# Performance work log

Hardware: AMD Instinct MI355X
Metric: run time of the kernel (lower is better)

Reference implementation:

```python
import jax, jax.numpy as jnp
import numpy as np

NUM_HEADS = 12

def setup_inputs() -> dict:
    key = jax.random.key(0)
    k1, k2, k3, k4 = jax.random.split(key, 4)
    B, N, C = 64, 197, 768
    x = jax.random.normal(k1, (B, N, C), dtype=jnp.float32)
    w_qkv = jax.random.normal(k2, (3 * C, C), dtype=jnp.float32) * (C ** -0.5)
    w_proj = jax.random.normal(k3, (C, C), dtype=jnp.float32) * (C ** -0.5)
    b_proj = jax.random.normal(k4, (C,), dtype=jnp.float32) * 0.01
    return {"x": x, "w_qkv": w_qkv, "w_proj": w_proj, "b_proj": b_proj}

def reference(x, w_qkv, w_proj, b_proj):
    B, N, C = x.shape
    H = NUM_HEADS
    hd = C // H
    scale = hd ** -0.5
    # qkv linear (no bias): [B,N,3C] -> [3,B,H,N,hd]
    qkv = jnp.einsum('bnc,dc->bnd', x, w_qkv).reshape(B, N, 3, H, hd)
    qkv = jnp.transpose(qkv, (2, 0, 3, 1, 4))
    q, k, v = qkv[0], qkv[1], qkv[2]
    # full attention matrix [B,H,N,N] (materialized, matching the original)
    attn = jax.nn.softmax(jnp.einsum('bhnd,bhmd->bhnm', q, k) * scale, axis=-1)
    # CLS-token attention stats: mean over heads of attn row 0 (patch tokens) -> [B, N-1]
    global_attn = jnp.mean(attn[:, :, 0, 1:], axis=1)
    out = jnp.einsum('bhnm,bhmd->bhnd', attn, v)          # [B,H,N,hd]
    out = jnp.transpose(out, (0, 2, 1, 3)).reshape(B, N, C)
    out = jnp.einsum('bnc,dc->bnd', out, w_proj) + b_proj
    return out, global_attn
```

## Files before the change

### kernel.cpp

```cpp
#include <hip/hip_runtime.h>
#include <math.h>

#define B_   64
#define N_   197
#define C_   768
#define H_   12
#define HD_  64
#define BH_  (B_ * H_)
#define M_   (B_ * N_)

typedef _Float16 half8 __attribute__((ext_vector_type(8)));
typedef float    f32x4 __attribute__((ext_vector_type(4)));

#define XH_OFF   0u
#define WQH_OFF  19365888u
#define WPH_OFF  22904832u
#define QH_OFF   24084480u
#define KH_OFF   43450368u
#define VH_OFF   62816256u
#define OH_OFF   82182144u
#define P0_OFF   101548032u
#define WS_BYTES 102150144u

__device__ __forceinline__ half8 h8zero() {
    half8 z;
    #pragma unroll
    for (int i = 0; i < 8; ++i) z[i] = (_Float16)0;
    return z;
}

__device__ __forceinline__ void async16(const _Float16* g, _Float16* l) {
    __builtin_amdgcn_global_load_lds(
        (const __attribute__((address_space(1))) void*)g,
        (__attribute__((address_space(3))) void*)l,
        16, 0, 0);
}

__device__ __forceinline__ int xcd_swz(int i, int nwg) {
    const int q = nwg >> 3, r = nwg & 7;
    const int xcd = i & 7, j = i >> 3;
    return (xcd < r ? xcd * (q + 1) : r * (q + 1) + (xcd - r) * q) + j;
}

__global__ void k_ws_too_small(float* out, float ws_bytes) { out[0] = -ws_bytes; }

__global__ __launch_bounds__(256) void k_cvt_all(const float* __restrict__ x,
                                                 const float* __restrict__ wq,
                                                 const float* __restrict__ wp,
                                                 _Float16* __restrict__ Xh,
                                                 _Float16* __restrict__ Wqh,
                                                 _Float16* __restrict__ Wph) {
    int i = blockIdx.x * blockDim.x + threadIdx.x;
    const float* src;
    _Float16*    dst;
    if (i < 1210368)      { src = x;  dst = Xh; }
    else if (i < 1431552) { src = wq; dst = Wqh; i -= 1210368; }
    else                  { src = wp; dst = Wph; i -= 1431552; }
    float4 f0 = *(const float4*)(src + (size_t)i * 8);
    float4 f1 = *(const float4*)(src + (size_t)i * 8 + 4);
    half8 h;
    h[0]=(_Float16)f0.x; h[1]=(_Float16)f0.y; h[2]=(_Float16)f0.z; h[3]=(_Float16)f0.w;
    h[4]=(_Float16)f1.x; h[5]=(_Float16)f1.y; h[6]=(_Float16)f1.z; h[7]=(_Float16)f1.w;
    *(half8*)(dst + (size_t)i * 8) = h;
}

__device__ __forceinline__ void mfma_nt_core_h(const _Float16* __restrict__ A,
                                               const _Float16* __restrict__ B,
                                               int M, int K, int m0, int n0,
                                               _Float16* As, _Float16* Bs,
                                               f32x4 (&acc)[4][4]) {
    const int tid  = threadIdx.x;
    const int wave = tid >> 6, lane = tid & 63;
    const int wr   = (wave >> 1) << 6;
    const int wc   = (wave & 1) << 6;
    const int ln   = lane & 15, kq = lane >> 4;

    const int row0 = tid >> 2;
    const int ch0  = (tid & 3) << 3;
    int ar0 = m0 + row0;        if (ar0 >= M) ar0 = 0;
    int ar1 = m0 + 64 + row0;   if (ar1 >= M) ar1 = 0;
    const _Float16* A0 = A + (size_t)ar0 * K + ch0;
    const _Float16* A1 = A + (size_t)ar1 * K + ch0;
    const _Float16* B0 = B + (size_t)(n0 + row0) * K + ch0;
    const _Float16* B1 = B + (size_t)(n0 + 64 + row0) * K + ch0;
    _Float16* AsD = As + (wave << 9);
    _Float16* BsD = Bs + (wave << 9);

    for (int k0 = 0; k0 < K; k0 += 32) {
        __syncthreads();
        async16(A0 + k0, AsD);
        async16(A1 + k0, AsD + 2048);
        async16(B0 + k0, BsD);
        async16(B1 + k0, BsD + 2048);
        __syncthreads();

        half8 af[4], bf[4];
        #pragma unroll
        for (int t = 0; t < 4; ++t) {
            af[t] = *(const half8*)&As[(wr + t * 16 + ln) * 32 + kq * 8];
            bf[t] = *(const half8*)&Bs[(wc + t * 16 + ln) * 32 + kq * 8];
        }
        #pragma unroll
        for (int i = 0; i < 4; ++i)
            #pragma unroll
            for (int j = 0; j < 4; ++j)
                acc[i][j] = __builtin_amdgcn_mfma_f32_16x16x32_f16(af[i], bf[j], acc[i][j], 0, 0, 0);
    }
}

__global__ __launch_bounds__(256) void k_qkv_mfma(const _Float16* __restrict__ Xh,
                                                  const _Float16* __restrict__ Wq,
                                                  _Float16* __restrict__ Qh,
                                                  _Float16* __restrict__ Kh,
                                                  _Float16* __restrict__ Vh) {
    __shared__ _Float16 As[128 * 32];
    __shared__ _Float16 Bs[128 * 32];
    const int work = xcd_swz(blockIdx.y * 18 + blockIdx.x, 18 * 99);
    const int m0 = (work / 18) << 7;
    const int n0 = (work % 18) << 7;
    f32x4 acc[4][4] = {};
    mfma_nt_core_h(Xh, Wq, M_, C_, m0, n0, As, Bs, acc);

    const int lane = threadIdx.x & 63;
    const int wave = threadIdx.x >> 6;
    const int wr = (wave >> 1) << 6, wc = (wave & 1) << 6;
    const int ln = lane & 15, kq = lane >> 4;

    _Float16* basep[4];
    float     scl[4];
    #pragma unroll
    for (int nt = 0; nt < 4; ++nt) {
        const int d  = n0 + wc + nt * 16 + ln;
        const int t3 = d / C_;
        const int rr = d - t3 * C_;
        const int h  = rr >> 6;
        const int e  = rr & 63;
        _Float16* t = (t3 == 0) ? Qh : (t3 == 1) ? Kh : Vh;
        basep[nt] = t + (size_t)h * N_ * HD_ + e;
        scl[nt]   = (t3 == 0) ? 0.125f : 1.f;
    }
    #pragma unroll
    for (int mt = 0; mt < 4; ++mt) {
        #pragma unroll
        for (int i = 0; i < 4; ++i) {
            const int m = m0 + wr + mt * 16 + kq * 4 + i;
            if (m >= M_) continue;
            const int b = m / N_;
            const int n = m - b * N_;
            const size_t rowoff = ((size_t)b * H_ * N_ + n) * HD_;
            #pragma unroll
            for (int nt = 0; nt < 4; ++nt)
                basep[nt][rowoff] = (_Float16)(acc[mt][nt][i] * scl[nt]);
        }
    }
}

__global__ __launch_bounds__(256) void k_proj_mfma(const _Float16* __restrict__ Oh,
                                                   const _Float16* __restrict__ Wp,
                                                   const float* __restrict__ bias,
                                                   float* __restrict__ out) {
    __shared__ _Float16 As[128 * 32];
    __shared__ _Float16 Bs[128 * 32];
    const int work = xcd_swz(blockIdx.y * 6 + blockIdx.x, 6 * 99);
    const int m0 = (work / 6) << 7;
    const int n0 = (work % 6) << 7;
    f32x4 acc[4][4] = {};
    mfma_nt_core_h(Oh, Wp, M_, C_, m0, n0, As, Bs, acc);

    const int lane = threadIdx.x & 63;
    const int wave = threadIdx.x >> 6;
    const int wr = (wave >> 1) << 6, wc = (wave & 1) << 6;
    const int ln = lane & 15, kq = lane >> 4;
    float bv[4];
    #pragma unroll
    for (int nt = 0; nt < 4; ++nt) bv[nt] = bias[n0 + wc + nt * 16 + ln];
    #pragma unroll
    for (int mt = 0; mt < 4; ++mt) {
        #pragma unroll
        for (int i = 0; i < 4; ++i) {
            const int m = m0 + wr + mt * 16 + kq * 4 + i;
            if (m >= M_) continue;
            #pragma unroll
            for (int nt = 0; nt < 4; ++nt)
                out[(size_t)m * C_ + n0 + wc + nt * 16 + ln] = acc[mt][nt][i] + bv[nt];
        }
    }
}

__global__ __launch_bounds__(256) void k_attn(const _Float16* __restrict__ Qh,
                                              const _Float16* __restrict__ Kh,
                                              const _Float16* __restrict__ Vh,
                                              _Float16* __restrict__ Oh,
                                              float* __restrict__ P0) {
    __shared__ _Float16 lds[29824];
    _Float16* Ks = lds;
    _Float16* Pl = lds;
    _Float16* Vt = lds + 14976;

    const int work = xcd_swz(blockIdx.y * 4 + blockIdx.x, 4 * BH_);
    const int bh = work >> 2, rt = work & 3;
    const int b = bh / H_, h = bh - b * H_;
    const int tid = threadIdx.x, wave = tid >> 6, lane = tid & 63;
    const int ln = lane & 15, kq = lane >> 4;
    const size_t kvb = (size_t)bh * N_ * HD_;

    for (int idx = tid; idx < 208 * 8; idx += 256) {
        const int key = idx >> 3, c = (idx & 7) << 3;
        half8 v = (key < N_) ? *(const half8*)(Kh + kvb + (size_t)key * HD_ + c) : h8zero();
        *(half8*)&Ks[key * 72 + c] = v;
    }
    for (int idx = tid; idx < 197 * 8; idx += 256) {
        const int key = idx >> 3, c = (idx & 7) << 3;
        half8 v = *(const half8*)(Vh + kvb + (size_t)key * HD_ + c);
        #pragma unroll
        for (int j = 0; j < 8; ++j) Vt[(c + j) * 232 + key] = v[j];
    }
    for (int idx = tid; idx < 64 * 27; idx += 256) {
        const int d = idx / 27, k = 197 + (idx - d * 27);
        Vt[d * 232 + k] = (_Float16)0;
    }
    const int qrow = rt * 64 + wave * 16 + ln;
    const _Float16* Qp = Qh + kvb + (size_t)((qrow < N_) ? qrow : 0) * HD_ + kq * 8;
    half8 qf0 = *(const half8*)Qp;
    half8 qf1 = *(const half8*)(Qp + 32);
    __syncthreads();

    f32x4 acc[13] = {};
    __builtin_amdgcn_s_setprio(1);
    #pragma unroll
    for (int c = 0; c < 13; ++c) {
        const _Float16* kp = &Ks[(c * 16 + ln) * 72 + kq * 8];
        half8 kf0 = *(const half8*)kp;
        half8 kf1 = *(const half8*)(kp + 32);
        acc[c] = __builtin_amdgcn_mfma_f32_16x16x32_f16(qf0, kf0, acc[c], 0, 0, 0);
        acc[c] = __builtin_amdgcn_mfma_f32_16x16x32_f16(qf1, kf1, acc[c], 0, 0, 0);
    }
    __builtin_amdgcn_s_setprio(0);
    float inv4[4];
    #pragma unroll
    for (int r = 0; r < 4; ++r) {
        float m = -1e30f;
        #pragma unroll
        for (int c = 0; c < 13; ++c) {
            float x = ((c * 16 + ln) < N_) ? acc[c][r] : -1e30f;
            acc[c][r] = x;
            m = fmaxf(m, x);
        }
        m = fmaxf(m, __shfl_xor(m, 1)); m = fmaxf(m, __shfl_xor(m, 2));
        m = fmaxf(m, __shfl_xor(m, 4)); m = fmaxf(m, __shfl_xor(m, 8));
        float s = 0.f;
        #pragma unroll
        for (int c = 0; c < 13; ++c) { float e = __expf(acc[c][r] - m); acc[c][r] = e; s += e; }
        s += __shfl_xor(s, 1); s += __shfl_xor(s, 2);
        s += __shfl_xor(s, 4); s += __shfl_xor(s, 8);
        inv4[r] = 1.f / s;
    }
    __syncthreads();

    _Float16* Pw = Pl + wave * 16 * 232;
    #pragma unroll
    for (int c = 0; c < 13; ++c) {
        const int col = c * 16 + ln;
        #pragma unroll
        for (int r = 0; r < 4; ++r)
            Pw[(kq * 4 + r) * 232 + col] = (_Float16)(acc[c][r] * inv4[r]);
    }
    #pragma unroll
    for (int r = 0; r < 4; ++r) Pw[(kq * 4 + r) * 232 + 208 + ln] = (_Float16)0;

    if (rt == 0 && wave == 0 && kq == 0) {
        #pragma unroll
        for (int c = 0; c < 13; ++c) {
            const int col = c * 16 + ln;
            if (col >= 1 && col < N_) P0[(size_t)bh * 196 + col - 1] = acc[c][0] * inv4[0];
        }
    }
    __syncthreads();

    f32x4 o4[4] = {};
    __builtin_amdgcn_s_setprio(1);
    for (int t = 0; t < 7; ++t) {
        half8 pf = *(const half8*)&Pw[ln * 232 + kq * 8 + 32 * t];
        #pragma unroll
        for (int n = 0; n < 4; ++n) {
            half8 vf = *(const half8*)&Vt[(n * 16 + ln) * 232 + kq * 8 + 32 * t];
            o4[n] = __builtin_amdgcn_mfma_f32_16x16x32_f16(pf, vf, o4[n], 0, 0, 0);
        }
    }
    __builtin_amdgcn_s_setprio(0);
    const int g0 = rt * 64 + wave * 16 + kq * 4;
    #pragma unroll
    for (int r = 0; r < 4; ++r) {
        const int g = g0 + r;
        if (g >= N_) continue;
        _Float16* op = Oh + ((size_t)b * N_ + g) * C_ + h * HD_;
        #pragma unroll
        for (int n = 0; n < 4; ++n) op[n * 16 + ln] = (_Float16)o4[n][r];
    }
}

__global__ void k_gattn(const float* __restrict__ P0, float* __restrict__ out2) {
    const int idx = blockIdx.x * blockDim.x + threadIdx.x;
    const int b = idx / (N_ - 1), m = idx - b * (N_ - 1);
    float s = 0.f;
    #pragma unroll
    for (int h = 0; h < H_; ++h) s += P0[((size_t)(b * H_ + h)) * 196 + m];
    out2[idx] = s * (1.f / H_);
}

extern "C" void kernel_launch(void* const* d_in, const int* in_sizes, int n_in,
                              void* d_out, int out_size, void* d_ws, size_t ws_size,
                              hipStream_t stream) {
    const float* x      = (const float*)d_in[0];
    const float* w_qkv  = (const float*)d_in[1];
    const float* w_proj = (const float*)d_in[2];
    const float* b_proj = (const float*)d_in[3];
    float* out = (float*)d_out;
    char* ws   = (char*)d_ws;

    if (ws_size < (size_t)WS_BYTES) {
        k_ws_too_small<<<1, 1, 0, stream>>>(out, (float)ws_size);
        return;
    }

    _Float16* Xh  = (_Float16*)(ws + XH_OFF);
    _Float16* Wqh = (_Float16*)(ws + WQH_OFF);
    _Float16* Wph = (_Float16*)(ws + WPH_OFF);
    _Float16* Qh  = (_Float16*)(ws + QH_OFF);
    _Float16* Kh  = (_Float16*)(ws + KH_OFF);
    _Float16* Vh  = (_Float16*)(ws + VH_OFF);
    _Float16* Oh  = (_Float16*)(ws + OH_OFF);
    float*    P0  = (float*)   (ws + P0_OFF);

    k_cvt_all<<<5880, 256, 0, stream>>>(x, w_qkv, w_proj, Xh, Wqh, Wph);

    k_qkv_mfma <<<dim3(18, 99), 256, 0, stream>>>(Xh, Wqh, Qh, Kh, Vh);
    k_attn     <<<dim3(4, BH_), 256, 0, stream>>>(Qh, Kh, Vh, Oh, P0);
    k_gattn    <<<dim3(49),     256, 0, stream>>>(P0, out + (size_t)M_ * C_);
    k_proj_mfma<<<dim3(6, 99),  256, 0, stream>>>(Oh, Wph, b_proj, out);
}
```

Measured before the change: 243.7 us.

## Rewrite GEMM core as 256x256 double-buffered tile with swizzled LDS

Replaces the 128x128, single-buffered GEMM core used by the QKV and projection kernels with a 256x256 tile over 8 waves and a K-step of 64. Global-to-LDS loads are double-buffered and interleaved with MFMA phases, using explicit waitcnt, barriers and setprio. LDS is XOR-swizzled to avoid bank conflicts. The aim is more data reuse per LDS load and load latency hidden behind compute. The cost is much higher LDS and register use per block, and with few blocks (450 and 150) and a partial last M tile, the GPU may not fill evenly.

```diff
diff --git a/kernel.cpp b/kernel.cpp
--- a/kernel.cpp
+++ b/kernel.cpp
@@ -64,125 +64,219 @@
     *(half8*)(dst + (size_t)i * 8) = h;
 }
 
-__device__ __forceinline__ void mfma_nt_core_h(const _Float16* __restrict__ A,
-                                               const _Float16* __restrict__ B,
-                                               int M, int K, int m0, int n0,
-                                               _Float16* As, _Float16* Bs,
-                                               f32x4 (&acc)[4][4]) {
+__device__ __forceinline__ void mfma_nt_core_256(const _Float16* __restrict__ A,
+                                                 const _Float16* __restrict__ B,
+                                                 int M, int K, int m0, int n0,
+                                                 _Float16* As, _Float16* Bs,
+                                                 f32x4 (&acc)[8][4]) {
     const int tid  = threadIdx.x;
-    const int wave = tid >> 6, lane = tid & 63;
-    const int wr   = (wave >> 1) << 6;
-    const int wc   = (wave & 1) << 6;
+    const int lane = tid & 63;
+    const int w    = tid >> 6;
+    const int wm   = w >> 2, wn = w & 3;
     const int ln   = lane & 15, kq = lane >> 4;
 
-    const int row0 = tid >> 2;
-    const int ch0  = (tid & 3) << 3;
-    int ar0 = m0 + row0;        if (ar0 >= M) ar0 = 0;
-    int ar1 = m0 + 64 + row0;   if (ar1 >= M) ar1 = 0;
-    const _Float16* A0 = A + (size_t)ar0 * K + ch0;
-    const _Float16* A1 = A + (size_t)ar1 * K + ch0;
-    const _Float16* B0 = B + (size_t)(n0 + row0) * K + ch0;
-    const _Float16* B1 = B + (size_t)(n0 + 64 + row0) * K + ch0;
-    _Float16* AsD = As + (wave << 9);
-    _Float16* BsD = Bs + (wave << 9);
-
-    for (int k0 = 0; k0 < K; k0 += 32) {
-        __syncthreads();
-        async16(A0 + k0, AsD);
-        async16(A1 + k0, AsD + 2048);
-        async16(B0 + k0, BsD);
-        async16(B1 + k0, BsD + 2048);
-        __syncthreads();
-
-        half8 af[4], bf[4];
-        #pragma unroll
-        for (int t = 0; t < 4; ++t) {
-            af[t] = *(const half8*)&As[(wr + t * 16 + ln) * 32 + kq * 8];
-            bf[t] = *(const half8*)&Bs[(wc + t * 16 + ln) * 32 + kq * 8];
-        }
-        #pragma unroll
-        for (int i = 0; i < 4; ++i)
-            #pragma unroll
-            for (int j = 0; j < 4; ++j)
-                acc[i][j] = __builtin_amdgcn_mfma_f32_16x16x32_f16(af[i], bf[j], acc[i][j], 0, 0, 0);
-    }
-}
-
-__global__ __launch_bounds__(256) void k_qkv_mfma(const _Float16* __restrict__ Xh,
-                                                  const _Float16* __restrict__ Wq,
-                                                  _Float16* __restrict__ Qh,
-                                                  _Float16* __restrict__ Kh,
-                                                  _Float16* __restrict__ Vh) {
-    __shared__ _Float16 As[128 * 32];
-    __shared__ _Float16 Bs[128 * 32];
-    const int work = xcd_swz(blockIdx.y * 18 + blockIdx.x, 18 * 99);
-    const int m0 = (work / 18) << 7;
-    const int n0 = (work % 18) << 7;
-    f32x4 acc[4][4] = {};
-    mfma_nt_core_h(Xh, Wq, M_, C_, m0, n0, As, Bs, acc);
+    const int srow = tid >> 3;
+    const int kcs  = (((tid & 7) ^ (srow & 7)) << 3);
+    int ra00 = m0 +       srow; if (ra00 >= M) ra00 = 0;
+    int ra01 = m0 +  64 + srow; if (ra01 >= M) ra01 = 0;
+    int ra10 = m0 + 128 + srow; if (ra10 >= M) ra10 = 0;
+    int ra11 = m0 + 192 + srow; if (ra11 >= M) ra11 = 0;
+    const _Float16* A00 = A + (size_t)ra00 * K + kcs;
+    const _Float16* A01 = A + (size_t)ra01 * K + kcs;
+    const _Float16* A10 = A + (size_t)ra10 * K + kcs;
+    const _Float16* A11 = A + (size_t)ra11 * K + kcs;
+    const _Float16* B00 = B + (size_t)(n0 +       srow) * K + kcs;
+    const _Float16* B01 = B + (size_t)(n0 +  64 + srow) * K + kcs;
+    const _Float16* B10 = B + (size_t)(n0 + 128 + srow) * K + kcs;
+    const _Float16* B11 = B + (size_t)(n0 + 192 + srow) * K + kcs;
+    const int dOff = w << 9;
+
+    const int kx    = (ln & 7) << 3;
+    const int aBase = wm * 8192 + ln * 64;
+    const int bBase = (wn >> 1) * 8192 + (wn & 1) * 4096 + ln * 64;
+
+    half8 af[4][2], bf[4][2];
+
+    async16(A00, As + dOff);          async16(A01, As + 4096 + dOff);
+    async16(A10, As + 8192 + dOff);   async16(A11, As + 12288 + dOff);
+    async16(B00, Bs + dOff);          async16(B01, Bs + 4096 + dOff);
+    async16(B10, Bs + 8192 + dOff);   async16(B11, Bs + 12288 + dOff);
+
+    const int NT = K >> 6;
+    #pragma unroll 1
+    for (int t = 0; t < NT; ++t) {
+        const int cur  = (t & 1) << 14;
+        const int nb   = 16384 - cur;
+        const int koff = (t + 1) << 6;
+        const bool pre = (t + 1 < NT);
+        const _Float16* Ac = As + cur;
+        const _Float16* Bc = Bs + cur;
+
+        if (pre) {
+            async16(A00 + koff, As + nb + dOff);
+            async16(A01 + koff, As + nb + 4096 + dOff);
+            async16(A10 + koff, As + nb + 8192 + dOff);
+            async16(A11 + koff, As + nb + 12288 + dOff);
+            asm volatile("s_waitcnt vmcnt(4)" ::: "memory");
+        } else {
+            asm volatile("s_waitcnt vmcnt(0)" ::: "memory");
+        }
+        __builtin_amdgcn_s_barrier();
+        __builtin_amdgcn_sched_barrier(0);
+        #pragma unroll
+        for (int m4 = 0; m4 < 4; ++m4)
+            #pragma unroll
+            for (int kk = 0; kk < 2; ++kk)
+                af[m4][kk] = *(const half8*)&Ac[aBase + m4 * 1024 + ((kk * 32 + kq * 8) ^ kx)];
+        #pragma unroll
+        for (int n2 = 0; n2 < 2; ++n2)
+            #pragma unroll
+            for (int kk = 0; kk < 2; ++kk)
+                bf[n2][kk] = *(const half8*)&Bc[bBase + n2 * 1024 + ((kk * 32 + kq * 8) ^ kx)];
+        __builtin_amdgcn_s_setprio(1);
+        #pragma unroll
+        for (int m4 = 0; m4 < 4; ++m4)
+            #pragma unroll
+            for (int n2 = 0; n2 < 2; ++n2)
+                #pragma unroll
+                for (int kk = 0; kk < 2; ++kk)
+                    acc[m4][n2] = __builtin_amdgcn_mfma_f32_16x16x32_f16(af[m4][kk], bf[n2][kk], acc[m4][n2], 0, 0, 0);
+        __builtin_amdgcn_s_setprio(0);
+        __builtin_amdgcn_sched_barrier(0);
+        __builtin_amdgcn_s_barrier();
+
+        if (pre) {
+            async16(B00 + koff, Bs + nb + dOff);
+            async16(B01 + koff, Bs + nb + 4096 + dOff);
+        }
+        #pragma unroll
+        for (int n2 = 0; n2 < 2; ++n2)
+            #pragma unroll
+            for (int kk = 0; kk < 2; ++kk)
+                bf[2 + n2][kk] = *(const half8*)&Bc[bBase + (2 + n2) * 1024 + ((kk * 32 + kq * 8) ^ kx)];
+        __builtin_amdgcn_s_setprio(1);
+        #pragma unroll
+        for (int m4 = 0; m4 < 4; ++m4)
+            #pragma unroll
+            for (int n2 = 0; n2 < 2; ++n2)
+                #pragma unroll
+                for (int kk = 0; kk < 2; ++kk)
+                    acc[m4][2 + n2] = __builtin_amdgcn_mfma_f32_16x16x32_f16(af[m4][kk], bf[2 + n2][kk], acc[m4][2 + n2], 0, 0, 0);
+        __builtin_amdgcn_s_setprio(0);
+        __builtin_amdgcn_sched_barrier(0);
+        __builtin_amdgcn_s_barrier();
+
+        if (pre) {
+            async16(B10 + koff, Bs + nb + 8192 + dOff);
+            async16(B11 + koff, Bs + nb + 12288 + dOff);
+        }
+        #pragma unroll
+        for (int m4 = 0; m4 < 4; ++m4)
+            #pragma unroll
+            for (int kk = 0; kk < 2; ++kk)
+                af[m4][kk] = *(const half8*)&Ac[aBase + (4 + m4) * 1024 + ((kk * 32 + kq * 8) ^ kx)];
+        __builtin_amdgcn_s_setprio(1);
+        #pragma unroll
+        for (int m4 = 0; m4 < 4; ++m4)
+            #pragma unroll
+            for (int n2 = 0; n2 < 2; ++n2)
+                #pragma unroll
+                for (int kk = 0; kk < 2; ++kk)
+                    acc[4 + m4][n2] = __builtin_amdgcn_mfma_f32_16x16x32_f16(af[m4][kk], bf[n2][kk], acc[4 + m4][n2], 0, 0, 0);
+        __builtin_amdgcn_s_setprio(0);
+        __builtin_amdgcn_sched_barrier(0);
+        __builtin_amdgcn_s_barrier();
+
+        __builtin_amdgcn_s_setprio(1);
+        #pragma unroll
+        for (int m4 = 0; m4 < 4; ++m4)
+            #pragma unroll
+            for (int n2 = 0; n2 < 2; ++n2)
+                #pragma unroll
+                for (int kk = 0; kk < 2; ++kk)
+                    acc[4 + m4][2 + n2] = __builtin_amdgcn_mfma_f32_16x16x32_f16(af[m4][kk], bf[2 + n2][kk], acc[4 + m4][2 + n2], 0, 0, 0);
+        __builtin_amdgcn_s_setprio(0);
+        asm volatile("s_waitcnt lgkmcnt(0)" ::: "memory");
+        __builtin_amdgcn_sched_barrier(0);
+        __builtin_amdgcn_s_barrier();
+    }
+}
+
+__global__ __launch_bounds__(512, 2) void k_qkv_mfma(const _Float16* __restrict__ Xh,
+                                                     const _Float16* __restrict__ Wq,
+                                                     _Float16* __restrict__ Qh,
+                                                     _Float16* __restrict__ Kh,
+                                                     _Float16* __restrict__ Vh) {
+    __shared__ _Float16 As[32768];
+    __shared__ _Float16 Bs[32768];
+    const int work = xcd_swz(blockIdx.x, 50 * 9);
+    const int m0 = (work / 9) << 8;
+    const int n0 = (work % 9) << 8;
+    f32x4 acc[8][4] = {};
+    mfma_nt_core_256(Xh, Wq, M_, C_, m0, n0, As, Bs, acc);
 
     const int lane = threadIdx.x & 63;
-    const int wave = threadIdx.x >> 6;
-    const int wr = (wave >> 1) << 6, wc = (wave & 1) << 6;
+    const int w    = threadIdx.x >> 6;
+    const int wm = w >> 2, wn = w & 3;
     const int ln = lane & 15, kq = lane >> 4;
 
     _Float16* basep[4];
     float     scl[4];
     #pragma unroll
-    for (int nt = 0; nt < 4; ++nt) {
-        const int d  = n0 + wc + nt * 16 + ln;
+    for (int ni = 0; ni < 4; ++ni) {
+        const int d  = n0 + wn * 64 + ni * 16 + ln;
         const int t3 = d / C_;
         const int rr = d - t3 * C_;
         const int h  = rr >> 6;
         const int e  = rr & 63;
-        _Float16* t = (t3 == 0) ? Qh : (t3 == 1) ? Kh : Vh;
-        basep[nt] = t + (size_t)h * N_ * HD_ + e;
-        scl[nt]   = (t3 == 0) ? 0.125f : 1.f;
-    }
-    #pragma unroll
-    for (int mt = 0; mt < 4; ++mt) {
+        _Float16* tp = (t3 == 0) ? Qh : (t3 == 1) ? Kh : Vh;
+        basep[ni] = tp + (size_t)h * N_ * HD_ + e;
+        scl[ni]   = (t3 == 0) ? 0.125f : 1.f;
+    }
+    #pragma unroll
+    for (int mi = 0; mi < 8; ++mi) {
         #pragma unroll
         for (int i = 0; i < 4; ++i) {
-            const int m = m0 + wr + mt * 16 + kq * 4 + i;
+            const int m = m0 + wm * 128 + mi * 16 + kq * 4 + i;
             if (m >= M_) continue;
             const int b = m / N_;
             const int n = m - b * N_;
             const size_t rowoff = ((size_t)b * H_ * N_ + n) * HD_;
             #pragma unroll
-            for (int nt = 0; nt < 4; ++nt)
-                basep[nt][rowoff] = (_Float16)(acc[mt][nt][i] * scl[nt]);
-        }
-    }
-}
-
-__global__ __launch_bounds__(256) void k_proj_mfma(const _Float16* __restrict__ Oh,
-                                                   const _Float16* __restrict__ Wp,
-                                                   const float* __restrict__ bias,
-                                                   float* __restrict__ out) {
-    __shared__ _Float16 As[128 * 32];
-    __shared__ _Float16 Bs[128 * 32];
-    const int work = xcd_swz(blockIdx.y * 6 + blockIdx.x, 6 * 99);
-    const int m0 = (work / 6) << 7;
-    const int n0 = (work % 6) << 7;
-    f32x4 acc[4][4] = {};
-    mfma_nt_core_h(Oh, Wp, M_, C_, m0, n0, As, Bs, acc);
+            for (int ni = 0; ni < 4; ++ni)
+                basep[ni][rowoff] = (_Float16)(acc[mi][ni][i] * scl[ni]);
+        }
+    }
+}
+
+__global__ __launch_bounds__(512, 2) void k_proj_mfma(const _Float16* __restrict__ Oh,
+                                                      const _Float16* __restrict__ Wp,
+                                                      const float* __restrict__ bias,
+                                                      float* __restrict__ out) {
+    __shared__ _Float16 As[32768];
+    __shared__ _Float16 Bs[32768];
+    const int work = xcd_swz(blockIdx.x, 50 * 3);
+    const int m0 = (work / 3) << 8;
+    const int n0 = (work % 3) << 8;
+    f32x4 acc[8][4] = {};
+    mfma_nt_core_256(Oh, Wp, M_, C_, m0, n0, As, Bs, acc);
 
     const int lane = threadIdx.x & 63;
-    const int wave = threadIdx.x >> 6;
-    const int wr = (wave >> 1) << 6, wc = (wave & 1) << 6;
+    const int w    = threadIdx.x >> 6;
+    const int wm = w >> 2, wn = w & 3;
     const int ln = lane & 15, kq = lane >> 4;
     float bv[4];
     #pragma unroll
-    for (int nt = 0; nt < 4; ++nt) bv[nt] = bias[n0 + wc + nt * 16 + ln];
-    #pragma unroll
-    for (int mt = 0; mt < 4; ++mt) {
+    for (int ni = 0; ni < 4; ++ni) bv[ni] = bias[n0 + wn * 64 + ni * 16 + ln];
+    #pragma unroll
+    for (int mi = 0; mi < 8; ++mi) {
         #pragma unroll
         for (int i = 0; i < 4; ++i) {
-            const int m = m0 + wr + mt * 16 + kq * 4 + i;
+            const int m = m0 + wm * 128 + mi * 16 + kq * 4 + i;
             if (m >= M_) continue;
             #pragma unroll
-            for (int nt = 0; nt < 4; ++nt)
-                out[(size_t)m * C_ + n0 + wc + nt * 16 + ln] = acc[mt][nt][i] + bv[nt];
+            for (int ni = 0; ni < 4; ++ni)
+                out[(size_t)m * C_ + n0 + wn * 64 + ni * 16 + ln] = acc[mi][ni][i] + bv[ni];
         }
     }
 }
@@ -334,8 +428,8 @@
 
     k_cvt_all<<<5880, 256, 0, stream>>>(x, w_qkv, w_proj, Xh, Wqh, Wph);
 
-    k_qkv_mfma <<<dim3(18, 99), 256, 0, stream>>>(Xh, Wqh, Qh, Kh, Vh);
+    k_qkv_mfma <<<dim3(450), 512, 0, stream>>>(Xh, Wqh, Qh, Kh, Vh);
     k_attn     <<<dim3(4, BH_), 256, 0, stream>>>(Qh, Kh, Vh, Oh, P0);
     k_gattn    <<<dim3(49),     256, 0, stream>>>(P0, out + (size_t)M_ * C_);
-    k_proj_mfma<<<dim3(6, 99),  256, 0, stream>>>(Oh, Wph, b_proj, out);
-}
+    k_proj_mfma<<<dim3(150), 512, 0, stream>>>(Oh, Wph, b_proj, out);
+}
```

New measurement: 249.7 us. 1.02x slower.
